# Performance work log

Measured on AMD Instinct MI355X. Metric: run time of the kernel, lower is better.

## Reference

```python
import jax, jax.numpy as jnp
import numpy as np

N_NODES = 100000
N_EDGES = 3200000
IN_DIM = 256
HID = 16
OUT = 10


def setup_inputs() -> dict:
    key = jax.random.key(0)
    k1, k2, k3, k4, k5, k6 = jax.random.split(key, 6)
    x = jax.random.normal(k1, (N_NODES, IN_DIM), dtype=jnp.float32)
    edge_index = jax.random.randint(k2, (2, N_EDGES), 0, N_NODES, dtype=jnp.int64)
    # Glorot-style init for GCN weights, zeros for bias (PyG defaults)
    W1 = jax.random.normal(k3, (IN_DIM, HID), dtype=jnp.float32) * (1.0 / np.sqrt(IN_DIM))
    b1 = jnp.zeros((HID,), dtype=jnp.float32)
    W2 = jax.random.normal(k4, (HID, OUT), dtype=jnp.float32) * (1.0 / np.sqrt(HID))
    b2 = jnp.zeros((OUT,), dtype=jnp.float32)
    return {"x": x, "edge_index": edge_index, "W1": W1, "b1": b1, "W2": W2, "b2": b2}


def _gcn_conv(h, src, dst, W, b, num_nodes):
    # GCNConv(normalize=False): out_i = sum_{(j->i) in E} (h_j W) + b
    m = h @ W                                   # [N, F_out] small GEMM
    agg = jax.ops.segment_sum(m[src], dst, num_segments=num_nodes)  # gather+scatter-add
    return agg + b


def reference(x, edge_index, W1, b1, W2, b2):
    src = edge_index[0]  # message source (flow: source_to_target)
    dst = edge_index[1]
    n = x.shape[0]
    h = jax.nn.relu(_gcn_conv(x, src, dst, W1, b1, n))
    # F.dropout with module in eval mode -> identity
    out = _gcn_conv(h, src, dst, W2, b2, n)
    return out
```

## Files before the change

kernel.cpp:

```cpp
#include <hip/hip_runtime.h>
#include <hip/hip_bf16.h>
#include <stdint.h>

#define IN_DIM 256
#define HID 16
#define OUTD 10
#define BKT_SHIFT 8
#define BKT_W 256
#define PART_CH 4096
#define EPT 16
#define G_HIST 512
#define SSRC_CAP 8704

typedef short v8s __attribute__((ext_vector_type(8)));
typedef float v4f __attribute__((ext_vector_type(4)));

__device__ __forceinline__ float bf2f(unsigned short u) {
    return __uint_as_float(((unsigned int)u) << 16);
}
__device__ __forceinline__ unsigned short f2bf(float f) {
    unsigned int u = __float_as_uint(f);
    unsigned int lsb = (u >> 16) & 1u;
    u += 0x7fffu + lsb;
    return (unsigned short)(u >> 16);
}

__device__ __forceinline__ int load_dst(const void* ei, int n_edges, int e, int is64) {
    return is64 ? (int)((const long long*)ei)[(size_t)n_edges + e]
                : ((const int*)ei)[(size_t)n_edges + e];
}
__device__ __forceinline__ int load_src(const void* ei, int n_edges, int e, int is64) {
    return is64 ? (int)((const long long*)ei)[e] : ((const int*)ei)[e];
}

__global__ void zero_kernel(int* __restrict__ bucket_cnt, int K) {
    for (int i = threadIdx.x; i < K; i += blockDim.x) bucket_cnt[i] = 0;
}

__global__ void setup_bhist_kernel(const void* __restrict__ x,
                                   const void* __restrict__ W1,
                                   const void* __restrict__ ei,
                                   int n_nodes, int n_edges,
                                   int* __restrict__ flags,
                                   int* __restrict__ bucket_cnt, int K,
                                   unsigned short* __restrict__ W1split) {
    __shared__ int lh[512];
    __shared__ int sflag;
    int b = blockIdx.x, t = threadIdx.x;

    if (b < 16) {
        if (t == 0) sflag = 0;
        __syncthreads();
        {
            float vw = bf2f(((const unsigned short*)W1)[t]);
            if (!(vw > -1e4f && vw < 1e4f)) sflag = 1;
        }
        __syncthreads();
        const int wf32 = sflag;
        int i = b * 256 + t;
        float w = wf32 ? ((const float*)W1)[i]
                       : bf2f(((const unsigned short*)W1)[i]);
        unsigned short hi = f2bf(w);
        unsigned short lo = f2bf(w - bf2f(hi));
        int k = i >> 4, n = i & 15;
        int kk = k >> 5, qd = (k >> 3) & 3, j = k & 7;
        int idx = ((kk * 4 + qd) * 16 + n) * 8 + j;
        W1split[idx] = hi;
        W1split[4096 + idx] = lo;
        return;
    }
    if (b == 16) {
        if (t < 64) {
            const unsigned short* xs = (const unsigned short*)x;
            const unsigned short* ws = (const unsigned short*)W1;
            bool badx = false, badw = false;
#pragma unroll
            for (int q = 0; q < 4; ++q) {
                float vx = bf2f(xs[t + 64 * q]);
                float vw = bf2f(ws[t + 64 * q]);
                if (!(vx > -1e4f && vx < 1e4f)) badx = true;
                if (!(vw > -1e4f && vw < 1e4f)) badw = true;
            }
            const unsigned long long* e64 = (const unsigned long long*)ei;
            bool big = false;
#pragma unroll
            for (int q = 0; q < 2; ++q)
                if (e64[t + 64 * q] >= (unsigned long long)n_nodes) big = true;
            int xf32 = __any(badx) ? 1 : 0;
            int wf32 = __any(badw) ? 1 : 0;
            int is64 = __any(big) ? 0 : 1;
            if (t == 0) { flags[0] = is64; flags[1] = xf32; flags[2] = wf32; }
        }
        return;
    }

    if (t == 0) sflag = 1;
    __syncthreads();
    {
        const unsigned long long* e64 = (const unsigned long long*)ei;
        if (t < 128 && e64[t] >= (unsigned long long)n_nodes) sflag = 0;
    }
    __syncthreads();
    const int is64 = sflag;
    for (int i = t; i < 512; i += 256) lh[i] = 0;
    __syncthreads();
    int vbid = b - 17;
    int stride = G_HIST * 256;
    for (int e = vbid * 256 + t; e < n_edges; e += stride) {
        int d = load_dst(ei, n_edges, e, is64);
        atomicAdd(&lh[d >> BKT_SHIFT], 1);
    }
    __syncthreads();
    for (int i = t; i < K; i += 256)
        if (lh[i]) atomicAdd(&bucket_cnt[i], lh[i]);
}

__global__ void bscan_kernel(const int* __restrict__ bucket_cnt, int K,
                             int* __restrict__ bucket_off, int* __restrict__ bcur,
                             int* __restrict__ row_off, int n_nodes, int n_edges) {
    __shared__ int ts[256];
    int t = threadIdx.x;
    const int KP = (K + 255) / 256;
    int base = t * KP;
    int local[8];
    int s = 0;
    for (int q = 0; q < KP; ++q) {
        int idx = base + q;
        int v = (idx < K) ? bucket_cnt[idx] : 0;
        local[q] = v; s += v;
    }
    ts[t] = s;
    __syncthreads();
    for (int off = 1; off < 256; off <<= 1) {
        int v = (t >= off) ? ts[t - off] : 0;
        __syncthreads();
        ts[t] += v;
        __syncthreads();
    }
    int ex = ts[t] - s;
    for (int q = 0; q < KP; ++q) {
        int idx = base + q;
        if (idx < K) { bucket_off[idx] = ex; bcur[idx] = ex; }
        ex += local[q];
    }
    if (t == 255) bucket_off[K] = ex;
    if (t == 0) row_off[n_nodes] = n_edges;
}

__global__ __launch_bounds__(256, 4) void part_gemm1_kernel(
        const void* __restrict__ ei, int n_edges,
        int* __restrict__ bcur, unsigned int* __restrict__ pairs,
        const void* __restrict__ xp_,
        const unsigned short* __restrict__ W1split,
        unsigned short* __restrict__ m1, int n_nodes,
        const int* __restrict__ flags, int K, int g_part) {
    __shared__ int lh[512];
    __shared__ int gdelta[512];
    __shared__ int ts[256];
    __shared__ unsigned int spairs[PART_CH];
    __shared__ unsigned short sbkt[PART_CH];
    int t = threadIdx.x;

    if ((int)blockIdx.x < g_part) {
        int begin = blockIdx.x * PART_CH;
        int is64 = flags[0];
        lh[t] = 0; lh[t + 256] = 0;

        int dloc[EPT];
#pragma unroll
        for (int i = 0; i < EPT; ++i) {
            int e = begin + i * 256 + t;
            dloc[i] = (e < n_edges) ? load_dst(ei, n_edges, e, is64) : -1;
        }
        __syncthreads();
#pragma unroll
        for (int i = 0; i < EPT; ++i)
            if (dloc[i] >= 0) atomicAdd(&lh[dloc[i] >> BKT_SHIFT], 1);
        __syncthreads();

        int c0 = lh[2 * t], c1 = lh[2 * t + 1];
        int s = c0 + c1;
        ts[t] = s;
        __syncthreads();
        for (int off = 1; off < 256; off <<= 1) {
            int v = (t >= off) ? ts[t - off] : 0;
            __syncthreads();
            ts[t] += v;
            __syncthreads();
        }
        int ex = ts[t] - s;
        if (c0 > 0) gdelta[2 * t]     = atomicAdd(&bcur[2 * t], c0) - ex;
        if (c1 > 0) gdelta[2 * t + 1] = atomicAdd(&bcur[2 * t + 1], c1) - (ex + c0);
        __syncthreads();
        lh[2 * t] = ex; lh[2 * t + 1] = ex + c0;
        __syncthreads();

#pragma unroll
        for (int i = 0; i < EPT; ++i) {
            int e = begin + i * 256 + t;
            if (dloc[i] >= 0) {
                int srcv = load_src(ei, n_edges, e, is64);
                int bb = dloc[i] >> BKT_SHIFT;
                int lpos = atomicAdd(&lh[bb], 1);
                spairs[lpos] = ((unsigned)srcv << 8) | ((unsigned)dloc[i] & (BKT_W - 1));
                sbkt[lpos] = (unsigned short)bb;
            }
        }
        __syncthreads();

        int total = n_edges - begin; if (total > PART_CH) total = PART_CH;
        for (int j = t; j < total; j += 256)
            pairs[gdelta[sbkt[j]] + j] = spairs[j];
        return;
    }

    const int xf32 = flags[1];
    int vb = blockIdx.x - g_part;
    int g_gemm = gridDim.x - g_part;
    int lane = t & 63;
    int wave = t >> 6;
    int col  = lane & 15;
    int quad = lane >> 4;
    int n_tiles = (n_nodes + 15) >> 4;
    const unsigned short* Whi = W1split;
    const unsigned short* Wlo = W1split + 4096;

    if (!xf32) {
        const unsigned short* x = (const unsigned short*)xp_;
        for (int tile = vb * 4 + wave; tile < n_tiles; tile += g_gemm * 4) {
            int row = tile * 16 + col;
            int r = row < n_nodes ? row : n_nodes - 1;
            const unsigned short* xp = x + (size_t)r * IN_DIM + quad * 8;
            v8s a[8];
#pragma unroll
            for (int kk = 0; kk < 8; ++kk)
                a[kk] = *(const v8s*)(xp + kk * 32);
            v4f acc1 = {0.f, 0.f, 0.f, 0.f};
            v4f acc2 = {0.f, 0.f, 0.f, 0.f};
#pragma unroll
            for (int kk = 0; kk < 8; ++kk) {
                v8s bh = *(const v8s*)&Whi[(kk * 64 + lane) * 8];
                v8s bl = *(const v8s*)&Wlo[(kk * 64 + lane) * 8];
                acc1 = __builtin_amdgcn_mfma_f32_16x16x32_bf16(a[kk], bh, acc1, 0, 0, 0);
                acc2 = __builtin_amdgcn_mfma_f32_16x16x32_bf16(a[kk], bl, acc2, 0, 0, 0);
            }
#pragma unroll
            for (int rg = 0; rg < 4; ++rg) {
                int node = tile * 16 + quad * 4 + rg;
                if (node < n_nodes)
                    m1[(size_t)node * HID + col] = f2bf(acc1[rg] + acc2[rg]);
            }
        }
    } else {
        const float* x = (const float*)xp_;
        for (int tile = vb * 4 + wave; tile < n_tiles; tile += g_gemm * 4) {
            int row = tile * 16 + col;
            int r = row < n_nodes ? row : n_nodes - 1;
            const float* xp = x + (size_t)r * IN_DIM + quad * 8;
            float4 u[16];
#pragma unroll
            for (int kk = 0; kk < 8; ++kk) {
                u[2 * kk]     = *(const float4*)(xp + kk * 32);
                u[2 * kk + 1] = *(const float4*)(xp + kk * 32 + 4);
            }
            v4f acc1 = {0.f, 0.f, 0.f, 0.f};
            v4f acc2 = {0.f, 0.f, 0.f, 0.f};
#pragma unroll
            for (int kk = 0; kk < 8; ++kk) {
                float uv[8] = {u[2 * kk].x,     u[2 * kk].y,
                               u[2 * kk].z,     u[2 * kk].w,
                               u[2 * kk + 1].x, u[2 * kk + 1].y,
                               u[2 * kk + 1].z, u[2 * kk + 1].w};
                v8s ahi, alo;
#pragma unroll
                for (int j = 0; j < 8; ++j) {
                    unsigned short hi = f2bf(uv[j]);
                    unsigned short lo = f2bf(uv[j] - bf2f(hi));
                    ahi[j] = (short)hi; alo[j] = (short)lo;
                }
                v8s bh = *(const v8s*)&Whi[(kk * 64 + lane) * 8];
                v8s bl = *(const v8s*)&Wlo[(kk * 64 + lane) * 8];
                acc1 = __builtin_amdgcn_mfma_f32_16x16x32_bf16(ahi, bh, acc1, 0, 0, 0);
                acc2 = __builtin_amdgcn_mfma_f32_16x16x32_bf16(ahi, bl, acc2, 0, 0, 0);
                acc2 = __builtin_amdgcn_mfma_f32_16x16x32_bf16(alo, bh, acc2, 0, 0, 0);
            }
#pragma unroll
            for (int rg = 0; rg < 4; ++rg) {
                int node = tile * 16 + quad * 4 + rg;
                if (node < n_nodes)
                    m1[(size_t)node * HID + col] = f2bf(acc1[rg] + acc2[rg]);
            }
        }
    }
}

__global__ __launch_bounds__(512) void csr_agg1_kernel(
        const unsigned int* __restrict__ pairs,
        const int* __restrict__ bucket_off,
        const unsigned short* __restrict__ m1,
        const void* __restrict__ b1p,
        int* __restrict__ row_off, int* __restrict__ csr_src,
        unsigned short* __restrict__ h,
        int n_nodes, const int* __restrict__ flags) {
    __shared__ unsigned int ssrc[SSRC_CAP];
    __shared__ int deg[BKT_W];
    __shared__ int cur[BKT_W];
    __shared__ int ts[BKT_W];
    int blk = blockIdx.x;
    int nbase = blk << BKT_SHIFT;
    int NL = n_nodes - nbase; if (NL > BKT_W) NL = BKT_W;
    int beg = bucket_off[blk], end = bucket_off[blk + 1];
    int t = threadIdx.x;

    if (t < BKT_W) deg[t] = 0;
    __syncthreads();
    for (int k = beg + t; k < end; k += 512)
        atomicAdd(&deg[pairs[k] & (BKT_W - 1)], 1);
    __syncthreads();
    if (t < BKT_W) ts[t] = deg[t];
    __syncthreads();
    for (int off = 1; off < BKT_W; off <<= 1) {
        int v = 0;
        if (t < BKT_W && t >= off) v = ts[t - off];
        __syncthreads();
        if (t < BKT_W) ts[t] += v;
        __syncthreads();
    }
    if (t < BKT_W) {
        int exl = ts[t] - deg[t];
        cur[t] = exl;
        if (t < NL) row_off[nbase + t] = beg + exl;
    }
    __syncthreads();
    for (int k = beg + t; k < end; k += 512) {
        unsigned int pr = pairs[k];
        int dl = pr & (BKT_W - 1);
        int pos = atomicAdd(&cur[dl], 1);
        int src = (int)(pr >> 8);
        csr_src[beg + pos] = src;
        if (pos < SSRC_CAP) ssrc[pos] = (unsigned)src;
    }
    __syncthreads();

    const int wf32 = flags[2];
    int q = t & 3, grp = t >> 2;
    float b0, b1v, b2v, b3;
    if (wf32) {
        const float* b = (const float*)b1p + q * 4;
        b0 = b[0]; b1v = b[1]; b2v = b[2]; b3 = b[3];
    } else {
        const unsigned short* b = (const unsigned short*)b1p + q * 4;
        b0 = bf2f(b[0]); b1v = bf2f(b[1]); b2v = bf2f(b[2]); b3 = bf2f(b[3]);
    }
    for (int nl = grp; nl < NL; nl += 128) {
        int sL = ts[nl] - deg[nl];
        int eL = ts[nl];
        float a0 = 0.f, a1 = 0.f, a2 = 0.f, a3 = 0.f;
        int k = sL;
        for (; k + 8 <= eL; k += 8) {
            int sidx[8];
            uint2 v[8];
#pragma unroll
            for (int u = 0; u < 8; ++u)
                sidx[u] = (k + u < SSRC_CAP) ? (int)ssrc[k + u]
                                             : csr_src[beg + k + u];
#pragma unroll
            for (int u = 0; u < 8; ++u)
                v[u] = *(const uint2*)(m1 + (size_t)sidx[u] * HID + q * 4);
#pragma unroll
            for (int u = 0; u < 8; ++u) {
                a0 += bf2f((unsigned short)(v[u].x));
                a1 += bf2f((unsigned short)(v[u].x >> 16));
                a2 += bf2f((unsigned short)(v[u].y));
                a3 += bf2f((unsigned short)(v[u].y >> 16));
            }
        }
        for (; k < eL; ++k) {
            int s = (k < SSRC_CAP) ? (int)ssrc[k] : csr_src[beg + k];
            uint2 v = *(const uint2*)(m1 + (size_t)s * HID + q * 4);
            a0 += bf2f((unsigned short)(v.x));
            a1 += bf2f((unsigned short)(v.x >> 16));
            a2 += bf2f((unsigned short)(v.y));
            a3 += bf2f((unsigned short)(v.y >> 16));
        }
        float r0 = fmaxf(a0 + b0, 0.f);
        float r1 = fmaxf(a1 + b1v, 0.f);
        float r2 = fmaxf(a2 + b2v, 0.f);
        float r3 = fmaxf(a3 + b3, 0.f);
        uint2 packed;
        packed.x = (unsigned int)f2bf(r0) | ((unsigned int)f2bf(r1) << 16);
        packed.y = (unsigned int)f2bf(r2) | ((unsigned int)f2bf(r3) << 16);
        *(uint2*)(h + (size_t)(nbase + nl) * HID + q * 4) = packed;
    }
}

__device__ __forceinline__ v4f gather_bf16(const unsigned short* __restrict__ src,
                                           const int* __restrict__ csr_src,
                                           int beg, int end, int q) {
    float a0 = 0.f, a1 = 0.f, a2 = 0.f, a3 = 0.f;
    int k = beg;
    for (; k + 16 <= end; k += 16) {
        uint2 v[16];
#pragma unroll
        for (int u = 0; u < 16; ++u) {
            int s = csr_src[k + u];
            v[u] = *(const uint2*)(src + (size_t)s * HID + q * 4);
        }
#pragma unroll
        for (int u = 0; u < 16; ++u) {
            a0 += bf2f((unsigned short)(v[u].x));
            a1 += bf2f((unsigned short)(v[u].x >> 16));
            a2 += bf2f((unsigned short)(v[u].y));
            a3 += bf2f((unsigned short)(v[u].y >> 16));
        }
    }
    for (; k + 4 <= end; k += 4) {
        uint2 v[4];
#pragma unroll
        for (int u = 0; u < 4; ++u) {
            int s = csr_src[k + u];
            v[u] = *(const uint2*)(src + (size_t)s * HID + q * 4);
        }
#pragma unroll
        for (int u = 0; u < 4; ++u) {
            a0 += bf2f((unsigned short)(v[u].x));
            a1 += bf2f((unsigned short)(v[u].x >> 16));
            a2 += bf2f((unsigned short)(v[u].y));
            a3 += bf2f((unsigned short)(v[u].y >> 16));
        }
    }
    for (; k < end; ++k) {
        int s = csr_src[k];
        uint2 v = *(const uint2*)(src + (size_t)s * HID + q * 4);
        a0 += bf2f((unsigned short)(v.x));
        a1 += bf2f((unsigned short)(v.x >> 16));
        a2 += bf2f((unsigned short)(v.y));
        a3 += bf2f((unsigned short)(v.y >> 16));
    }
    v4f r = {a0, a1, a2, a3};
    return r;
}

__global__ void agg2_out_kernel(const unsigned short* __restrict__ h,
                                const int* __restrict__ row_off,
                                const int* __restrict__ csr_src,
                                const void* __restrict__ W2p,
                                const void* __restrict__ b2p,
                                void* __restrict__ out, int n_nodes,
                                const int* __restrict__ flags) {
    __shared__ float Ws[HID * OUTD];
    __shared__ float bs[OUTD];
    const int xf32 = flags[1], wf32 = flags[2];
    if (threadIdx.x < HID * OUTD)
        Ws[threadIdx.x] = wf32 ? ((const float*)W2p)[threadIdx.x]
                               : bf2f(((const unsigned short*)W2p)[threadIdx.x]);
    if (threadIdx.x < OUTD)
        bs[threadIdx.x] = wf32 ? ((const float*)b2p)[threadIdx.x]
                               : bf2f(((const unsigned short*)b2p)[threadIdx.x]);
    __syncthreads();

    int t = blockIdx.x * blockDim.x + threadIdx.x;
    int node = t >> 2;
    if (node >= n_nodes) return;
    int q = t & 3;
    v4f a = gather_bf16(h, csr_src, row_off[node], row_off[node + 1], q);

    float o[OUTD];
#pragma unroll
    for (int od = 0; od < OUTD; ++od) {
        float s = 0.f;
#pragma unroll
        for (int j = 0; j < 4; ++j)
            s = fmaf(a[j], Ws[(q * 4 + j) * OUTD + od], s);
        o[od] = s;
    }
#pragma unroll
    for (int od = 0; od < OUTD; ++od) {
        o[od] += __shfl_xor(o[od], 1);
        o[od] += __shfl_xor(o[od], 2);
        o[od] += bs[od];
    }

    if (xf32) {
        float2* po = (float2*)((float*)out + (size_t)node * OUTD);
        if (q == 0) {
            po[0] = make_float2(o[0], o[1]);
            po[1] = make_float2(o[2], o[3]);
        } else if (q == 1) {
            po[2] = make_float2(o[4], o[5]);
            po[3] = make_float2(o[6], o[7]);
        } else if (q == 2) {
            po[4] = make_float2(o[8], o[9]);
        }
    } else {
        unsigned int* po = (unsigned int*)((unsigned short*)out + (size_t)node * OUTD);
        if (q == 0) {
            po[0] = (unsigned int)f2bf(o[0]) | ((unsigned int)f2bf(o[1]) << 16);
            po[1] = (unsigned int)f2bf(o[2]) | ((unsigned int)f2bf(o[3]) << 16);
        } else if (q == 1) {
            po[2] = (unsigned int)f2bf(o[4]) | ((unsigned int)f2bf(o[5]) << 16);
            po[3] = (unsigned int)f2bf(o[6]) | ((unsigned int)f2bf(o[7]) << 16);
        } else if (q == 2) {
            po[4] = (unsigned int)f2bf(o[8]) | ((unsigned int)f2bf(o[9]) << 16);
        }
    }
}

__global__ void sentinel_kernel(float* __restrict__ out) {
    if (blockIdx.x == 0 && threadIdx.x < 16) out[threadIdx.x] = 123456.0f;
}

extern "C" void kernel_launch(void* const* d_in, const int* in_sizes, int n_in,
                              void* d_out, int out_size, void* d_ws, size_t ws_size,
                              hipStream_t stream) {
    const void* x  = d_in[0];
    const void* ei = d_in[1];
    const void* W1 = d_in[2];
    const void* b1 = d_in[3];
    const void* W2 = d_in[4];
    const void* b2 = d_in[5];

    const int n_nodes = in_sizes[0] / IN_DIM;
    const int n_edges = in_sizes[1] / 2;
    const int K = (n_nodes + BKT_W - 1) / BKT_W;

    char* p = (char*)d_ws;
    auto align = [](size_t v) { return (v + 255) & ~(size_t)255; };
    size_t off = 0;
    int* flags      = (int*)(p + off); off = align(off + 256);
    unsigned short* w1split = (unsigned short*)(p + off); off = align(off + 8192 * 2);
    int* bucket_cnt = (int*)(p + off); off = align(off + (size_t)K * 4);
    int* bucket_off = (int*)(p + off); off = align(off + ((size_t)K + 1) * 4);
    int* bcur       = (int*)(p + off); off = align(off + (size_t)K * 4);
    int* row_off    = (int*)(p + off); off = align(off + ((size_t)n_nodes + 1) * 4);
    int* csr_src    = (int*)(p + off); off = align(off + (size_t)n_edges * 4);
    unsigned int* pairs = (unsigned int*)(p + off); off = align(off + (size_t)n_edges * 4);
    unsigned short* m1 = (unsigned short*)(p + off); off = align(off + (size_t)n_nodes * HID * 2);
    unsigned short* h  = (unsigned short*)(p + off); off = align(off + (size_t)n_nodes * HID * 2);

    if (ws_size < off) {
        sentinel_kernel<<<1, 64, 0, stream>>>((float*)d_out);
        return;
    }

    const int n_tiles16 = (n_nodes + 15) >> 4;
    const int g_gemm = (n_tiles16 + 3) / 4;
    const int g_part = (n_edges + PART_CH - 1) / PART_CH;

    zero_kernel<<<1, 256, 0, stream>>>(bucket_cnt, K);

    setup_bhist_kernel<<<17 + G_HIST, 256, 0, stream>>>(
        x, W1, ei, n_nodes, n_edges, flags, bucket_cnt, K, w1split);

    bscan_kernel<<<1, 256, 0, stream>>>(bucket_cnt, K, bucket_off, bcur,
                                        row_off, n_nodes, n_edges);

    part_gemm1_kernel<<<g_part + g_gemm, 256, 0, stream>>>(
        ei, n_edges, bcur, pairs, x, w1split, m1, n_nodes, flags, K, g_part);

    csr_agg1_kernel<<<K, 512, 0, stream>>>(pairs, bucket_off, m1, b1,
                                           row_off, csr_src, h, n_nodes, flags);

    {
        long long threads = (long long)n_nodes * 4;
        agg2_out_kernel<<<(int)((threads + 255) / 256), 256, 0, stream>>>(
            h, row_off, csr_src, W2, b2, d_out, n_nodes, flags);
    }
}
```

Baseline: 311.3 us.

## Fuse both aggregation layers into one cooperative kernel with grid sync

Adds a cooperative kernel that builds the per-bucket source list in shared memory once, runs the layer-1 aggregation with ReLU, then does a grid-wide sync and reuses the same shared CSR to run the layer-2 aggregation with the W2 projection. This removes one kernel launch and the separate global CSR used by the second layer's gather. The old two-kernel path is kept as a fallback if the cooperative launch fails. It requires all K=391 blocks of 512 threads to be co-resident and adds a grid barrier. The old kernels' unrolled loops were also trimmed.

```diff
diff --git a/kernel.cpp b/kernel.cpp
--- a/kernel.cpp
+++ b/kernel.cpp
@@ -1,6 +1,9 @@
 #include <hip/hip_runtime.h>
 #include <hip/hip_bf16.h>
+#include <hip/hip_cooperative_groups.h>
 #include <stdint.h>
+
+namespace cg = cooperative_groups;
 
 #define IN_DIM 256
 #define HID 16
@@ -11,6 +14,7 @@
 #define EPT 16
 #define G_HIST 512
 #define SSRC_CAP 8704
+#define SSRC_CAP2 9216
 
 typedef short v8s __attribute__((ext_vector_type(8)));
 typedef float v4f __attribute__((ext_vector_type(4)));
@@ -289,6 +293,191 @@
                 int node = tile * 16 + quad * 4 + rg;
                 if (node < n_nodes)
                     m1[(size_t)node * HID + col] = f2bf(acc1[rg] + acc2[rg]);
+            }
+        }
+    }
+}
+
+__global__ __launch_bounds__(512, 4) void csr_agg12_kernel(
+        const unsigned int* __restrict__ pairs,
+        const int* __restrict__ bucket_off,
+        const unsigned short* __restrict__ m1,
+        const void* __restrict__ b1p,
+        const void* __restrict__ W2p,
+        const void* __restrict__ b2p,
+        int* __restrict__ spill,
+        unsigned short* __restrict__ h,
+        void* __restrict__ out,
+        int n_nodes, const int* __restrict__ flags) {
+    __shared__ int deg[BKT_W];
+    __shared__ int cur[BKT_W];
+    __shared__ int ts[BKT_W];
+    __shared__ float wsb[192];
+    __shared__ unsigned int ssrc[SSRC_CAP2];
+    cg::grid_group grid = cg::this_grid();
+
+    int blk = blockIdx.x;
+    int nbase = blk << BKT_SHIFT;
+    int NL = n_nodes - nbase; if (NL > BKT_W) NL = BKT_W; if (NL < 0) NL = 0;
+    int beg = bucket_off[blk], end = bucket_off[blk + 1];
+    int t = threadIdx.x;
+    const int xf32 = flags[1], wf32 = flags[2];
+
+    if (t < HID * OUTD)
+        wsb[t] = wf32 ? ((const float*)W2p)[t] : bf2f(((const unsigned short*)W2p)[t]);
+    if (t >= 256 && t < 256 + OUTD) {
+        int i = t - 256;
+        wsb[160 + i] = wf32 ? ((const float*)b2p)[i] : bf2f(((const unsigned short*)b2p)[i]);
+    }
+    if (t >= 288 && t < 288 + HID) {
+        int i = t - 288;
+        wsb[176 + i] = wf32 ? ((const float*)b1p)[i] : bf2f(((const unsigned short*)b1p)[i]);
+    }
+    if (t < BKT_W) deg[t] = 0;
+    __syncthreads();
+
+    for (int k = beg + t; k < end; k += 512)
+        atomicAdd(&deg[pairs[k] & (BKT_W - 1)], 1);
+    __syncthreads();
+    if (t < BKT_W) ts[t] = deg[t];
+    __syncthreads();
+    for (int off = 1; off < BKT_W; off <<= 1) {
+        int v = 0;
+        if (t < BKT_W && t >= off) v = ts[t - off];
+        __syncthreads();
+        if (t < BKT_W) ts[t] += v;
+        __syncthreads();
+    }
+    if (t < BKT_W) cur[t] = ts[t] - deg[t];
+    __syncthreads();
+    for (int k = beg + t; k < end; k += 512) {
+        unsigned int pr = pairs[k];
+        int dl = pr & (BKT_W - 1);
+        int pos = atomicAdd(&cur[dl], 1);
+        int src = (int)(pr >> 8);
+        if (pos < SSRC_CAP2) ssrc[pos] = (unsigned)src;
+        else spill[beg + pos] = src;
+    }
+    __syncthreads();
+
+    int q = t & 3, grp = t >> 2;
+    {
+        float b0 = wsb[176 + q * 4 + 0], b1v = wsb[176 + q * 4 + 1];
+        float b2v = wsb[176 + q * 4 + 2], b3 = wsb[176 + q * 4 + 3];
+        for (int nl = grp; nl < NL; nl += 128) {
+            int sL = ts[nl] - deg[nl];
+            int eL = ts[nl];
+            float a0 = 0.f, a1 = 0.f, a2 = 0.f, a3 = 0.f;
+            int k = sL;
+            for (; k + 8 <= eL; k += 8) {
+                int sidx[8];
+                uint2 v[8];
+#pragma unroll
+                for (int u = 0; u < 8; ++u)
+                    sidx[u] = (k + u < SSRC_CAP2) ? (int)ssrc[k + u]
+                                                  : spill[beg + k + u];
+#pragma unroll
+                for (int u = 0; u < 8; ++u)
+                    v[u] = *(const uint2*)(m1 + (size_t)sidx[u] * HID + q * 4);
+#pragma unroll
+                for (int u = 0; u < 8; ++u) {
+                    a0 += bf2f((unsigned short)(v[u].x));
+                    a1 += bf2f((unsigned short)(v[u].x >> 16));
+                    a2 += bf2f((unsigned short)(v[u].y));
+                    a3 += bf2f((unsigned short)(v[u].y >> 16));
+                }
+            }
+            for (; k < eL; ++k) {
+                int s = (k < SSRC_CAP2) ? (int)ssrc[k] : spill[beg + k];
+                uint2 v = *(const uint2*)(m1 + (size_t)s * HID + q * 4);
+                a0 += bf2f((unsigned short)(v.x));
+                a1 += bf2f((unsigned short)(v.x >> 16));
+                a2 += bf2f((unsigned short)(v.y));
+                a3 += bf2f((unsigned short)(v.y >> 16));
+            }
+            float r0 = fmaxf(a0 + b0, 0.f);
+            float r1 = fmaxf(a1 + b1v, 0.f);
+            float r2 = fmaxf(a2 + b2v, 0.f);
+            float r3 = fmaxf(a3 + b3, 0.f);
+            uint2 packed;
+            packed.x = (unsigned int)f2bf(r0) | ((unsigned int)f2bf(r1) << 16);
+            packed.y = (unsigned int)f2bf(r2) | ((unsigned int)f2bf(r3) << 16);
+            *(uint2*)(h + (size_t)(nbase + nl) * HID + q * 4) = packed;
+        }
+    }
+
+    __threadfence();
+    grid.sync();
+
+    for (int nl = grp; nl < NL; nl += 128) {
+        int sL = ts[nl] - deg[nl];
+        int eL = ts[nl];
+        float a0 = 0.f, a1 = 0.f, a2 = 0.f, a3 = 0.f;
+        int k = sL;
+        for (; k + 8 <= eL; k += 8) {
+            int sidx[8];
+            uint2 v[8];
+#pragma unroll
+            for (int u = 0; u < 8; ++u)
+                sidx[u] = (k + u < SSRC_CAP2) ? (int)ssrc[k + u]
+                                              : spill[beg + k + u];
+#pragma unroll
+            for (int u = 0; u < 8; ++u)
+                v[u] = *(const uint2*)(h + (size_t)sidx[u] * HID + q * 4);
+#pragma unroll
+            for (int u = 0; u < 8; ++u) {
+                a0 += bf2f((unsigned short)(v[u].x));
+                a1 += bf2f((unsigned short)(v[u].x >> 16));
+                a2 += bf2f((unsigned short)(v[u].y));
+                a3 += bf2f((unsigned short)(v[u].y >> 16));
+            }
+        }
+        for (; k < eL; ++k) {
+            int s = (k < SSRC_CAP2) ? (int)ssrc[k] : spill[beg + k];
+            uint2 v = *(const uint2*)(h + (size_t)s * HID + q * 4);
+            a0 += bf2f((unsigned short)(v.x));
+            a1 += bf2f((unsigned short)(v.x >> 16));
+            a2 += bf2f((unsigned short)(v.y));
+            a3 += bf2f((unsigned short)(v.y >> 16));
+        }
+        float av[4] = {a0, a1, a2, a3};
+        float o[OUTD];
+#pragma unroll
+        for (int od = 0; od < OUTD; ++od) {
+            float s = 0.f;
+#pragma unroll
+            for (int j = 0; j < 4; ++j)
+                s = fmaf(av[j], wsb[(q * 4 + j) * OUTD + od], s);
+            o[od] = s;
+        }
+#pragma unroll
+        for (int od = 0; od < OUTD; ++od) {
+            o[od] += __shfl_xor(o[od], 1);
+            o[od] += __shfl_xor(o[od], 2);
+            o[od] += wsb[160 + od];
+        }
+        int node = nbase + nl;
+        if (xf32) {
+            float2* po = (float2*)((float*)out + (size_t)node * OUTD);
+            if (q == 0) {
+                po[0] = make_float2(o[0], o[1]);
+                po[1] = make_float2(o[2], o[3]);
+            } else if (q == 1) {
+                po[2] = make_float2(o[4], o[5]);
+                po[3] = make_float2(o[6], o[7]);
+            } else if (q == 2) {
+                po[4] = make_float2(o[8], o[9]);
+            }
+        } else {
+            unsigned int* po = (unsigned int*)((unsigned short*)out + (size_t)node * OUTD);
+            if (q == 0) {
+                po[0] = (unsigned int)f2bf(o[0]) | ((unsigned int)f2bf(o[1]) << 16);
+                po[1] = (unsigned int)f2bf(o[2]) | ((unsigned int)f2bf(o[3]) << 16);
+            } else if (q == 1) {
+                po[2] = (unsigned int)f2bf(o[4]) | ((unsigned int)f2bf(o[5]) << 16);
+                po[3] = (unsigned int)f2bf(o[6]) | ((unsigned int)f2bf(o[7]) << 16);
+            } else if (q == 2) {
+                po[4] = (unsigned int)f2bf(o[8]) | ((unsigned int)f2bf(o[9]) << 16);
             }
         }
     }
@@ -356,26 +545,7 @@
         int sL = ts[nl] - deg[nl];
         int eL = ts[nl];
         float a0 = 0.f, a1 = 0.f, a2 = 0.f, a3 = 0.f;
-        int k = sL;
-        for (; k + 8 <= eL; k += 8) {
-            int sidx[8];
-            uint2 v[8];
-#pragma unroll
-            for (int u = 0; u < 8; ++u)
-                sidx[u] = (k + u < SSRC_CAP) ? (int)ssrc[k + u]
-                                             : csr_src[beg + k + u];
-#pragma unroll
-            for (int u = 0; u < 8; ++u)
-                v[u] = *(const uint2*)(m1 + (size_t)sidx[u] * HID + q * 4);
-#pragma unroll
-            for (int u = 0; u < 8; ++u) {
-                a0 += bf2f((unsigned short)(v[u].x));
-                a1 += bf2f((unsigned short)(v[u].x >> 16));
-                a2 += bf2f((unsigned short)(v[u].y));
-                a3 += bf2f((unsigned short)(v[u].y >> 16));
-            }
-        }
-        for (; k < eL; ++k) {
+        for (int k = sL; k < eL; ++k) {
             int s = (k < SSRC_CAP) ? (int)ssrc[k] : csr_src[beg + k];
             uint2 v = *(const uint2*)(m1 + (size_t)s * HID + q * 4);
             a0 += bf2f((unsigned short)(v.x));
@@ -408,21 +578,6 @@
         }
 #pragma unroll
         for (int u = 0; u < 16; ++u) {
-            a0 += bf2f((unsigned short)(v[u].x));
-            a1 += bf2f((unsigned short)(v[u].x >> 16));
-            a2 += bf2f((unsigned short)(v[u].y));
-            a3 += bf2f((unsigned short)(v[u].y >> 16));
-        }
-    }
-    for (; k + 4 <= end; k += 4) {
-        uint2 v[4];
-#pragma unroll
-        for (int u = 0; u < 4; ++u) {
-            int s = csr_src[k + u];
-            v[u] = *(const uint2*)(src + (size_t)s * HID + q * 4);
-        }
-#pragma unroll
-        for (int u = 0; u < 4; ++u) {
             a0 += bf2f((unsigned short)(v[u].x));
             a1 += bf2f((unsigned short)(v[u].x >> 16));
             a2 += bf2f((unsigned short)(v[u].y));
@@ -558,12 +713,32 @@
     part_gemm1_kernel<<<g_part + g_gemm, 256, 0, stream>>>(
         ei, n_edges, bcur, pairs, x, w1split, m1, n_nodes, flags, K, g_part);
 
-    csr_agg1_kernel<<<K, 512, 0, stream>>>(pairs, bucket_off, m1, b1,
-                                           row_off, csr_src, h, n_nodes, flags);
-
     {
-        long long threads = (long long)n_nodes * 4;
-        agg2_out_kernel<<<(int)((threads + 255) / 256), 256, 0, stream>>>(
-            h, row_off, csr_src, W2, b2, d_out, n_nodes, flags);
-    }
-}
+        const unsigned int* pairs_c = pairs;
+        const int* bucket_off_c = bucket_off;
+        const unsigned short* m1_c = m1;
+        const void* b1_c = b1;
+        const void* W2_c = W2;
+        const void* b2_c = b2;
+        int* spill_c = csr_src;
+        unsigned short* h_c = h;
+        void* out_c = d_out;
+        int n_nodes_c = n_nodes;
+        const int* flags_c = flags;
+        void* args[] = {
+            (void*)&pairs_c, (void*)&bucket_off_c, (void*)&m1_c,
+            (void*)&b1_c, (void*)&W2_c, (void*)&b2_c,
+            (void*)&spill_c, (void*)&h_c, (void*)&out_c,
+            (void*)&n_nodes_c, (void*)&flags_c
+        };
+        hipError_t err = hipLaunchCooperativeKernel(
+            (const void*)csr_agg12_kernel, dim3(K), dim3(512), args, 0, stream);
+        if (err != hipSuccess) {
+            csr_agg1_kernel<<<K, 512, 0, stream>>>(
+                pairs, bucket_off, m1, b1, row_off, csr_src, h, n_nodes, flags);
+            long long threads = (long long)n_nodes * 4;
+            agg2_out_kernel<<<(int)((threads + 255) / 256), 256, 0, stream>>>(
+                h, row_off, csr_src, W2, b2, d_out, n_nodes, flags);
+        }
+    }
+}
```

Result: slower. 433.8 us (+39.4%).
